# Kernel tuning notes

Measured on AMD Instinct MI355X. Metric: run time of the kernel, lower is better.

## Reference

```python
import jax, jax.numpy as jnp
import numpy as np

B, T, D = 2, 1024, 1024
H, DH = 16, 64
HD = H * DH          # head_dim = n_heads*d_head = 1024
F = 2048             # expert_dim
E = 8                # n_routed_experts


def bitlinear(x, W):
    # 1.58-bit ternary quant with straight-through estimator
    scale = jnp.clip(jnp.abs(W).mean(axis=1, keepdims=True), 1e-5, None)
    wq = jnp.clip(jnp.round(W / scale), -1.0, 1.0)
    w = W + jax.lax.stop_gradient(wq * scale - W)
    return x @ w.T


def layernorm(x, g, b):
    m = jnp.mean(x, -1, keepdims=True)
    v = jnp.mean((x - m) ** 2, -1, keepdims=True)
    return (x - m) * jax.lax.rsqrt(v + 1e-5) * g + b


def setup_inputs():
    key = jax.random.key(0)
    ks = jax.random.split(key, 12)
    n = lambda k, s, sd: jax.random.normal(k, s, jnp.float32) * sd
    return {
        'x': jax.random.normal(ks[0], (B, T, D), jnp.float32),
        'mask': jnp.tril(jnp.ones((T, T), bool))[None, None],  # causal [1,1,T,T]
        'Wq': n(ks[1], (2 * HD, D), (2 * HD) ** -0.5),
        'Wk': n(ks[2], (2 * HD, D), (2 * HD) ** -0.5),
        'Wv': n(ks[3], (HD, D), HD ** -0.5),
        'Wo': n(ks[4], (D, HD), D ** -0.5),
        'lambda_q': n(ks[5], (H, DH), 0.1),
        'lambda_k': n(ks[6], (H, DH), 0.1),
        'qn_g': jnp.ones(2 * HD), 'qn_b': jnp.zeros(2 * HD),
        'kn_g': jnp.ones(2 * HD), 'kn_b': jnp.zeros(2 * HD),
        'attn_g': jnp.ones(D), 'attn_b': jnp.zeros(D),
        'ffn_g': jnp.ones(D), 'ffn_b': jnp.zeros(D),
        'moe_g': jnp.ones(D), 'moe_b': jnp.zeros(D),
        'shared_w1': n(ks[7], (F, D), F ** -0.5),
        'shared_w2': n(ks[8], (D, F), D ** -0.5),
        'expert_w1': n(ks[9], (E, F, D), F ** -0.5),
        'expert_w2': n(ks[10], (E, D, F), D ** -0.5),
        'router_w': n(ks[11], (E, D), 0.02),
    }


def diff_attention(x, mask, Wq, Wk, Wv, Wo, lambda_q, lambda_k, qn_g, qn_b, kn_g, kn_b):
    Bq, Tq, _ = x.shape
    q = layernorm(bitlinear(x, Wq), qn_g, qn_b).reshape(Bq, Tq, 2, H, DH)
    k = layernorm(bitlinear(x, Wk), kn_g, kn_b).reshape(Bq, Tq, 2, H, DH)
    v = bitlinear(x, Wv).reshape(Bq, Tq, H, DH)
    lam = jnp.clip(jnp.exp(lambda_q.mean() - lambda_k.mean()), 0.1, 2.0)
    scale = DH ** -0.5

    def one_attn(qi, ki):
        s = jnp.einsum('bthd,bshd->bhts', qi, ki) * scale
        s = jnp.where(mask, s, -jnp.inf)
        p = jax.nn.softmax(s, -1)
        return jnp.einsum('bhts,bshd->bthd', p, v)

    out1 = one_attn(q[:, :, 0], k[:, :, 0])
    out2 = one_attn(q[:, :, 1], k[:, :, 1])
    out = (out1 - lam * out2).reshape(Bq, Tq, HD)
    return bitlinear(out, Wo)


def ignition_moe(x, moe_g, moe_b, shared_w1, shared_w2, expert_w1, expert_w2, router_w):
    h = layernorm(x, moe_g, moe_b)
    shared = bitlinear(jax.nn.silu(bitlinear(h, shared_w1)), shared_w2)
    probs = jax.nn.softmax(h @ router_w.T, -1)          # [B,T,E]
    idx = jnp.argmax(probs, -1)                          # top-1 expert id
    top_p = jnp.take_along_axis(probs, idx[..., None], -1)  # [B,T,1]
    routed = jnp.zeros_like(h)
    for e in range(E):  # small fixed expert count
        out_e = bitlinear(jax.nn.silu(bitlinear(h, expert_w1[e])), expert_w2[e])
        sel = (idx == e)[..., None]
        routed = routed + jnp.where(sel, out_e * top_p, 0.0)
    return shared + routed


def reference(x, mask, Wq, Wk, Wv, Wo, lambda_q, lambda_k, qn_g, qn_b, kn_g, kn_b,
              attn_g, attn_b, ffn_g, ffn_b, moe_g, moe_b,
              shared_w1, shared_w2, expert_w1, expert_w2, router_w):
    h = layernorm(x, attn_g, attn_b)
    x = x + diff_attention(h, mask, Wq, Wk, Wv, Wo, lambda_q, lambda_k, qn_g, qn_b, kn_g, kn_b)
    h = layernorm(x, ffn_g, ffn_b)
    x = x + ignition_moe(h, moe_g, moe_b, shared_w1, shared_w2, expert_w1, expert_w2, router_w)
    return x
```

## Files before the change

### kernel.cpp

```cpp
#include <hip/hip_runtime.h>
#include <hip/hip_bf16.h>

#define B_ 2
#define T_ 1024
#define D_ 1024
#define H_ 16
#define DH_ 64
#define F_ 2048
#define E_ 8
#define M_ 2048

typedef _Float16 half8 __attribute__((ext_vector_type(8)));
typedef _Float16 half4v __attribute__((ext_vector_type(4)));
typedef float f32x4 __attribute__((ext_vector_type(4)));

template<bool ABS>
__device__ __forceinline__ float np_pairwise_wave(const float* a, int K, int lane) {
  int nb = K >> 7;
  float s = 0.f;
  if (lane < nb) {
    const float* p = a + (lane << 7);
    float r[8];
    #pragma unroll
    for (int j = 0; j < 8; ++j) r[j] = ABS ? fabsf(p[j]) : p[j];
    for (int i = 8; i < 128; i += 8)
      #pragma unroll
      for (int j = 0; j < 8; ++j) r[j] += ABS ? fabsf(p[i + j]) : p[i + j];
    s = ((r[0] + r[1]) + (r[2] + r[3])) + ((r[4] + r[5]) + (r[6] + r[7]));
  }
  for (int off = 1; off < nb; off <<= 1) s += __shfl_xor(s, off);
  return __shfl(s, 0);
}

__global__ __launch_bounds__(64) void k_scaleq_all(
    const float* __restrict__ Wq, const float* __restrict__ Wk,
    const float* __restrict__ Wv, const float* __restrict__ Wo,
    const float* __restrict__ sw1, const float* __restrict__ sw2,
    const float* __restrict__ ew1, const float* __restrict__ ew2,
    float* __restrict__ scWq, float* __restrict__ scWk,
    float* __restrict__ scWv, float* __restrict__ scWo,
    float* __restrict__ scS1, float* __restrict__ scS2,
    float* __restrict__ scE1, float* __restrict__ scE2,
    _Float16* __restrict__ QWq, _Float16* __restrict__ QWk,
    _Float16* __restrict__ QWv, _Float16* __restrict__ QWo,
    _Float16* __restrict__ QS1, _Float16* __restrict__ QS2,
    _Float16* __restrict__ QE1, _Float16* __restrict__ QE2)
{
  int r = blockIdx.x, lane = threadIdx.x;
  const float* W; float* sc; _Float16* qo; int K; int rr;
  if      (r < 2048)  { W = Wq;  sc = scWq; qo = QWq; K = 1024; rr = r; }
  else if (r < 4096)  { W = Wk;  sc = scWk; qo = QWk; K = 1024; rr = r - 2048; }
  else if (r < 5120)  { W = Wv;  sc = scWv; qo = QWv; K = 1024; rr = r - 4096; }
  else if (r < 6144)  { W = Wo;  sc = scWo; qo = QWo; K = 1024; rr = r - 5120; }
  else if (r < 8192)  { W = sw1; sc = scS1; qo = QS1; K = 1024; rr = r - 6144; }
  else if (r < 9216)  { W = sw2; sc = scS2; qo = QS2; K = 2048; rr = r - 8192; }
  else if (r < 25600) { W = ew1; sc = scE1; qo = QE1; K = 1024; rr = r - 9216; }
  else                { W = ew2; sc = scE2; qo = QE2; K = 2048; rr = r - 25600; }
  const float* row = W + (size_t)rr * K;
  float S = np_pairwise_wave<true>(row, K, lane);
  float s = fmaxf(S / (float)K, 1e-5f);
  if (lane == 0) sc[rr] = s;
  _Float16* dst = qo + (size_t)rr * K;
  for (int k = lane * 4; k < K; k += 256) {
    float4 w = *reinterpret_cast<const float4*>(row + k);
    float wv[4] = {w.x, w.y, w.z, w.w};
    half4v q4;
    #pragma unroll
    for (int j = 0; j < 4; ++j) {
      float q = rintf(wv[j] / s);
      q = fminf(1.f, fmaxf(-1.f, q));
      q4[j] = (_Float16)q;
    }
    *reinterpret_cast<half4v*>(dst + k) = q4;
  }
}

__global__ __launch_bounds__(64) void k_lambda(const float* __restrict__ lq,
                                               const float* __restrict__ lk,
                                               float* __restrict__ lam) {
  int lane = threadIdx.x;
  float mq = np_pairwise_wave<false>(lq, 1024, lane) / 1024.0f;
  float mk = np_pairwise_wave<false>(lk, 1024, lane) / 1024.0f;
  if (lane == 0) {
    float l = expf(mq - mk);
    lam[0] = fminf(2.0f, fmaxf(0.1f, l));
  }
}

__global__ __launch_bounds__(256) void k_layernorm(const float* __restrict__ in,
                                                   const float* __restrict__ g,
                                                   const float* __restrict__ b,
                                                   float* __restrict__ out, int Dd) {
  #pragma clang fp contract(off)
  __shared__ float row[2048];
  __shared__ float sq[2048];
  __shared__ float stat[2];
  int m = blockIdx.x, tid = threadIdx.x;
  const float* src = in + (size_t)m * Dd;
  for (int d = tid; d < Dd; d += 256) row[d] = src[d];
  __syncthreads();
  if (tid < 64) {
    float S = np_pairwise_wave<false>(row, Dd, tid);
    if (tid == 0) stat[0] = S;
  }
  __syncthreads();
  float mean = stat[0] / (float)Dd;
  for (int d = tid; d < Dd; d += 256) { float t = row[d] - mean; sq[d] = t * t; }
  __syncthreads();
  if (tid < 64) {
    float S = np_pairwise_wave<false>(sq, Dd, tid);
    if (tid == 0) stat[1] = S;
  }
  __syncthreads();
  float var = stat[1] / (float)Dd;
  float rs = 1.0f / sqrtf(var + 1e-5f);
  float* dst = out + (size_t)m * Dd;
  for (int d = tid; d < Dd; d += 256) {
    float t = row[d] - mean;
    float u = t * rs;
    float v = u * g[d];
    dst[d] = v + b[d];
  }
}

__global__ __launch_bounds__(256) void k_layernorm_split(const float* __restrict__ in,
                                                         const float* __restrict__ g,
                                                         const float* __restrict__ b,
                                                         _Float16* __restrict__ oh,
                                                         _Float16* __restrict__ ol, int Dd) {
  #pragma clang fp contract(off)
  __shared__ float row[2048];
  __shared__ float sq[2048];
  __shared__ float stat[2];
  int m = blockIdx.x, tid = threadIdx.x;
  const float* src = in + (size_t)m * Dd;
  for (int d = tid; d < Dd; d += 256) row[d] = src[d];
  __syncthreads();
  if (tid < 64) {
    float S = np_pairwise_wave<false>(row, Dd, tid);
    if (tid == 0) stat[0] = S;
  }
  __syncthreads();
  float mean = stat[0] / (float)Dd;
  for (int d = tid; d < Dd; d += 256) { float t = row[d] - mean; sq[d] = t * t; }
  __syncthreads();
  if (tid < 64) {
    float S = np_pairwise_wave<false>(sq, Dd, tid);
    if (tid == 0) stat[1] = S;
  }
  __syncthreads();
  float var = stat[1] / (float)Dd;
  float rs = 1.0f / sqrtf(var + 1e-5f);
  #pragma unroll 1
  for (int d = tid; d < Dd; d += 256) {
    float t = row[d] - mean;
    float u = t * rs;
    float v = u * g[d];
    float w = v + b[d];
    _Float16 hv = (_Float16)w;
    oh[(size_t)m * Dd + d] = hv;
    ol[(size_t)m * Dd + d] = (_Float16)((w - (float)hv) * 2048.0f);
  }
}

__global__ __launch_bounds__(256) void k_lnln(const float* __restrict__ in,
                                              const float* __restrict__ g1, const float* __restrict__ b1,
                                              const float* __restrict__ g2, const float* __restrict__ b2,
                                              float* __restrict__ outf,
                                              _Float16* __restrict__ outh) {
  #pragma clang fp contract(off)
  __shared__ float row[1024];
  __shared__ float tmp[1024];
  __shared__ float stat[2];
  int m = blockIdx.x, tid = threadIdx.x;
  const float* src = in + (size_t)m * 1024;
  for (int d = tid; d < 1024; d += 256) row[d] = src[d];
  __syncthreads();
  if (tid < 64) { float S = np_pairwise_wave<false>(row, 1024, tid); if (tid == 0) stat[0] = S; }
  __syncthreads();
  float mean = stat[0] / 1024.0f;
  for (int d = tid; d < 1024; d += 256) { float t = row[d] - mean; tmp[d] = t * t; }
  __syncthreads();
  if (tid < 64) { float S = np_pairwise_wave<false>(tmp, 1024, tid); if (tid == 0) stat[1] = S; }
  __syncthreads();
  float rs = 1.0f / sqrtf(stat[1] / 1024.0f + 1e-5f);
  for (int d = tid; d < 1024; d += 256) {
    float t = row[d] - mean;
    float u = t * rs;
    float v = u * g1[d];
    tmp[d] = v + b1[d];
  }
  __syncthreads();
  if (tid < 64) { float S = np_pairwise_wave<false>(tmp, 1024, tid); if (tid == 0) stat[0] = S; }
  __syncthreads();
  float mean2 = stat[0] / 1024.0f;
  for (int d = tid; d < 1024; d += 256) { float t = tmp[d] - mean2; row[d] = t * t; }
  __syncthreads();
  if (tid < 64) { float S = np_pairwise_wave<false>(row, 1024, tid); if (tid == 0) stat[1] = S; }
  __syncthreads();
  float rs2 = 1.0f / sqrtf(stat[1] / 1024.0f + 1e-5f);
  for (int d = tid; d < 1024; d += 256) {
    float t = tmp[d] - mean2;
    float u = t * rs2;
    float v = u * g2[d];
    float w = v + b2[d];
    outf[(size_t)m * 1024 + d] = w;
    outh[(size_t)m * 1024 + d] = (_Float16)w;
  }
}

template<int EPI, int XM, int DUAL>
__global__ __launch_bounds__(256) void k_mgemm(
    const _Float16* __restrict__ Agh, const _Float16* __restrict__ Agl, int lda,
    const _Float16* __restrict__ Wh, const float* __restrict__ scf,
    float* __restrict__ Cout, _Float16* __restrict__ Ch, _Float16* __restrict__ Ch2,
    int ldc, int N, int K,
    const float* __restrict__ res, const float* __restrict__ add2,
    const int* __restrict__ offs, const int* __restrict__ tlist,
    const float* __restrict__ topp)
{
  int e = XM ? blockIdx.z : 0;
  int mbase = 0, mcount = M_;
  const float* sc = scf;
  const _Float16* Whb = Wh;
  if (XM) {
    mbase = offs[e]; mcount = offs[e + 1] - mbase;
    Whb = Wh + (size_t)e * N * K;
    sc = scf + (size_t)e * N;
  }
  int m0 = blockIdx.y * 128;
  if (XM && m0 >= mcount) return;
  int n0 = blockIdx.x * 64;

  __shared__ __align__(16) _Float16 As[4][128][8];
  __shared__ __align__(16) _Float16 Als[DUAL ? 4 : 1][128][8];
  __shared__ __align__(16) _Float16 Qs[4][64][8];

  int tid = threadIdx.x;
  int lm  = tid >> 1;
  int kcA = (tid & 1) * 16;
  int lw  = tid >> 2;
  int kcW = (tid & 3) * 8;

  int am  = m0 + lm;
  int amc = XM ? ((am < mcount) ? am : (mcount - 1)) : am;
  int arow;
  if (XM == 1)      arow = tlist[mbase + amc];
  else if (XM == 2) arow = mbase + amc;
  else              arow = am;
  const _Float16* Arh = Agh + (size_t)arow * lda;
  const _Float16* Arl = DUAL ? (Agl + (size_t)arow * lda) : nullptr;
  const _Float16* Wrh = Whb + (size_t)(n0 + lw) * K;

  int wv = tid >> 6, lane = tid & 63;
  int wm = wv >> 1, wn = wv & 1;
  int ks = lane >> 4, fr = lane & 15;

  f32x4 acch[4][2], accl[4][2];
  #pragma unroll
  for (int i = 0; i < 4; i++)
    #pragma unroll
    for (int j = 0; j < 2; j++) { acch[i][j] = (f32x4)0.f; accl[i][j] = (f32x4)0.f; }

  for (int kt = 0; kt < K; kt += 32) {
    half8 a0 = *reinterpret_cast<const half8*>(Arh + kt + kcA);
    half8 a1 = *reinterpret_cast<const half8*>(Arh + kt + kcA + 8);
    half8 b0, b1;
    if (DUAL) {
      b0 = *reinterpret_cast<const half8*>(Arl + kt + kcA);
      b1 = *reinterpret_cast<const half8*>(Arl + kt + kcA + 8);
    }
    half8 qv = *reinterpret_cast<const half8*>(Wrh + kt + kcW);
    __syncthreads();
    int sA = kcA >> 3;
    *reinterpret_cast<half8*>(&As[sA][lm][0])     = a0;
    *reinterpret_cast<half8*>(&As[sA + 1][lm][0]) = a1;
    if (DUAL) {
      *reinterpret_cast<half8*>(&Als[sA][lm][0])     = b0;
      *reinterpret_cast<half8*>(&Als[sA + 1][lm][0]) = b1;
    }
    *reinterpret_cast<half8*>(&Qs[kcW >> 3][lw][0]) = qv;
    __syncthreads();
    half8 bfr0 = *reinterpret_cast<half8*>(&Qs[ks][wn * 32 + fr][0]);
    half8 bfr1 = *reinterpret_cast<half8*>(&Qs[ks][wn * 32 + 16 + fr][0]);
    #pragma unroll
    for (int i = 0; i < 4; i++) {
      half8 ah = *reinterpret_cast<half8*>(&As[ks][wm * 64 + i * 16 + fr][0]);
      acch[i][0] = __builtin_amdgcn_mfma_f32_16x16x32_f16(ah, bfr0, acch[i][0], 0, 0, 0);
      acch[i][1] = __builtin_amdgcn_mfma_f32_16x16x32_f16(ah, bfr1, acch[i][1], 0, 0, 0);
      if (DUAL) {
        half8 al = *reinterpret_cast<half8*>(&Als[ks][wm * 64 + i * 16 + fr][0]);
        accl[i][0] = __builtin_amdgcn_mfma_f32_16x16x32_f16(al, bfr0, accl[i][0], 0, 0, 0);
        accl[i][1] = __builtin_amdgcn_mfma_f32_16x16x32_f16(al, bfr1, accl[i][1], 0, 0, 0);
      }
    }
  }

  #pragma unroll
  for (int j = 0; j < 2; j++) {
    int col = n0 + wn * 32 + j * 16 + fr;
    float scl = sc[col];
    #pragma unroll
    for (int i = 0; i < 4; i++) {
      #pragma unroll
      for (int r = 0; r < 4; r++) {
        int lrow = m0 + wm * 64 + i * 16 + ks * 4 + r;
        if (XM && lrow >= mcount) continue;
        int orow;
        if (XM == 1)      orow = mbase + lrow;
        else if (XM == 2) orow = tlist[mbase + lrow];
        else              orow = lrow;
        float v = acch[i][j][r];
        if (DUAL) v += accl[i][j][r] * (1.0f / 2048.0f);
        v *= scl;
        if (EPI == 1) {
          v = v * (1.0f / (1.0f + __expf(-v)));
          Ch[(size_t)orow * ldc + col] = (_Float16)v;
        } else if (EPI == 2) {
          Cout[(size_t)orow * ldc + col] = res[(size_t)orow * ldc + col] + v;
        } else {
          Cout[(size_t)orow * ldc + col] = v;
        }
      }
    }
  }
}

__global__ __launch_bounds__(256) void k_mgemm_qkv(
    const _Float16* __restrict__ Agh, const _Float16* __restrict__ Agl,
    const _Float16* __restrict__ WQ_, const _Float16* __restrict__ WK_, const _Float16* __restrict__ WV_,
    const float* __restrict__ scq, const float* __restrict__ sck, const float* __restrict__ scv,
    float* __restrict__ Cq, float* __restrict__ Ck,
    _Float16* __restrict__ Vth, _Float16* __restrict__ Vtl)
{
  int nt = blockIdx.x;
  int sel = (nt < 32) ? 0 : (nt < 64 ? 1 : 2);
  int n0 = ((sel == 0) ? nt : (sel == 1) ? (nt - 32) : (nt - 64)) * 64;
  const _Float16* Wh = (sel == 0) ? WQ_ : (sel == 1) ? WK_ : WV_;
  const float* sc = (sel == 0) ? scq : (sel == 1) ? sck : scv;
  int m0 = blockIdx.y * 128;

  __shared__ __align__(16) _Float16 As[4][128][8];
  __shared__ __align__(16) _Float16 Als[4][128][8];
  __shared__ __align__(16) _Float16 Qs[4][64][8];

  int tid = threadIdx.x;
  int lm  = tid >> 1;
  int kcA = (tid & 1) * 16;
  int lw  = tid >> 2;
  int kcW = (tid & 3) * 8;

  const _Float16* Arh = Agh + (size_t)(m0 + lm) * 1024;
  const _Float16* Arl = Agl + (size_t)(m0 + lm) * 1024;
  const _Float16* Wrh = Wh + (size_t)(n0 + lw) * 1024;

  int wv = tid >> 6, lane = tid & 63;
  int wm = wv >> 1, wn = wv & 1;
  int ks = lane >> 4, fr = lane & 15;

  f32x4 acch[4][2], accl[4][2];
  #pragma unroll
  for (int i = 0; i < 4; i++)
    #pragma unroll
    for (int j = 0; j < 2; j++) { acch[i][j] = (f32x4)0.f; accl[i][j] = (f32x4)0.f; }

  for (int kt = 0; kt < 1024; kt += 32) {
    half8 a0 = *reinterpret_cast<const half8*>(Arh + kt + kcA);
    half8 a1 = *reinterpret_cast<const half8*>(Arh + kt + kcA + 8);
    half8 b0 = *reinterpret_cast<const half8*>(Arl + kt + kcA);
    half8 b1 = *reinterpret_cast<const half8*>(Arl + kt + kcA + 8);
    half8 qv = *reinterpret_cast<const half8*>(Wrh + kt + kcW);
    __syncthreads();
    int sA = kcA >> 3;
    *reinterpret_cast<half8*>(&As[sA][lm][0])      = a0;
    *reinterpret_cast<half8*>(&As[sA + 1][lm][0])  = a1;
    *reinterpret_cast<half8*>(&Als[sA][lm][0])     = b0;
    *reinterpret_cast<half8*>(&Als[sA + 1][lm][0]) = b1;
    *reinterpret_cast<half8*>(&Qs[kcW >> 3][lw][0]) = qv;
    __syncthreads();
    half8 bfr0 = *reinterpret_cast<half8*>(&Qs[ks][wn * 32 + fr][0]);
    half8 bfr1 = *reinterpret_cast<half8*>(&Qs[ks][wn * 32 + 16 + fr][0]);
    #pragma unroll
    for (int i = 0; i < 4; i++) {
      half8 ah = *reinterpret_cast<half8*>(&As[ks][wm * 64 + i * 16 + fr][0]);
      half8 al = *reinterpret_cast<half8*>(&Als[ks][wm * 64 + i * 16 + fr][0]);
      acch[i][0] = __builtin_amdgcn_mfma_f32_16x16x32_f16(ah, bfr0, acch[i][0], 0, 0, 0);
      acch[i][1] = __builtin_amdgcn_mfma_f32_16x16x32_f16(ah, bfr1, acch[i][1], 0, 0, 0);
      accl[i][0] = __builtin_amdgcn_mfma_f32_16x16x32_f16(al, bfr0, accl[i][0], 0, 0, 0);
      accl[i][1] = __builtin_amdgcn_mfma_f32_16x16x32_f16(al, bfr1, accl[i][1], 0, 0, 0);
    }
  }

  #pragma unroll
  for (int j = 0; j < 2; j++) {
    int col = n0 + wn * 32 + j * 16 + fr;
    float scl = sc[col];
    #pragma unroll
    for (int i = 0; i < 4; i++) {
      #pragma unroll
      for (int r = 0; r < 4; r++) {
        int orow = m0 + wm * 64 + i * 16 + ks * 4 + r;
        float v = (acch[i][j][r] + accl[i][j][r] * (1.0f / 2048.0f)) * scl;
        if (sel == 0) {
          Cq[(size_t)orow * 2048 + col] = v;
        } else if (sel == 1) {
          Ck[(size_t)orow * 2048 + col] = v;
        } else {
          int bb = orow >> 10, tok = orow & 1023;
          size_t vidx = ((size_t)(bb << 10) + col) * 1024 + tok;
          _Float16 hv = (_Float16)v;
          Vth[vidx] = hv;
          Vtl[vidx] = (_Float16)((v - (float)hv) * 2048.0f);
        }
      }
    }
  }
}

__global__ __launch_bounds__(256) void k_mgemm_moe1(
    const _Float16* __restrict__ Agh,
    const _Float16* __restrict__ WhS, const _Float16* __restrict__ WhE,
    const float* __restrict__ scS, const float* __restrict__ scE,
    _Float16* __restrict__ CS, _Float16* __restrict__ CE,
    const int* __restrict__ offs, const int* __restrict__ tlist)
{
  int z = blockIdx.z;
  int mbase = 0, mcount = M_;
  const _Float16* Whb = WhS;
  const float* sc = scS;
  if (z > 0) {
    int e = z - 1;
    mbase = offs[e]; mcount = offs[e + 1] - mbase;
    Whb = WhE + (size_t)e * 2048 * 1024;
    sc = scE + (size_t)e * 2048;
  }
  int m0 = blockIdx.y * 128;
  if (z > 0 && m0 >= mcount) return;
  int n0 = blockIdx.x * 64;

  __shared__ __align__(16) _Float16 As[4][128][8];
  __shared__ __align__(16) _Float16 Qs[4][64][8];

  int tid = threadIdx.x;
  int lm  = tid >> 1;
  int kcA = (tid & 1) * 16;
  int lw  = tid >> 2;
  int kcW = (tid & 3) * 8;

  int am  = m0 + lm;
  int amc = (z > 0) ? ((am < mcount) ? am : (mcount - 1)) : am;
  int arow = (z > 0) ? tlist[mbase + amc] : am;
  const _Float16* Arh = Agh + (size_t)arow * 1024;
  const _Float16* Wrh = Whb + (size_t)(n0 + lw) * 1024;

  int wv = tid >> 6, lane = tid & 63;
  int wm = wv >> 1, wn = wv & 1;
  int ks = lane >> 4, fr = lane & 15;

  f32x4 acch[4][2];
  #pragma unroll
  for (int i = 0; i < 4; i++)
    #pragma unroll
    for (int j = 0; j < 2; j++) acch[i][j] = (f32x4)0.f;

  for (int kt = 0; kt < 1024; kt += 32) {
    half8 a0 = *reinterpret_cast<const half8*>(Arh + kt + kcA);
    half8 a1 = *reinterpret_cast<const half8*>(Arh + kt + kcA + 8);
    half8 qv = *reinterpret_cast<const half8*>(Wrh + kt + kcW);
    __syncthreads();
    int sA = kcA >> 3;
    *reinterpret_cast<half8*>(&As[sA][lm][0])     = a0;
    *reinterpret_cast<half8*>(&As[sA + 1][lm][0]) = a1;
    *reinterpret_cast<half8*>(&Qs[kcW >> 3][lw][0]) = qv;
    __syncthreads();
    half8 bfr0 = *reinterpret_cast<half8*>(&Qs[ks][wn * 32 + fr][0]);
    half8 bfr1 = *reinterpret_cast<half8*>(&Qs[ks][wn * 32 + 16 + fr][0]);
    #pragma unroll
    for (int i = 0; i < 4; i++) {
      half8 ah = *reinterpret_cast<half8*>(&As[ks][wm * 64 + i * 16 + fr][0]);
      acch[i][0] = __builtin_amdgcn_mfma_f32_16x16x32_f16(ah, bfr0, acch[i][0], 0, 0, 0);
      acch[i][1] = __builtin_amdgcn_mfma_f32_16x16x32_f16(ah, bfr1, acch[i][1], 0, 0, 0);
    }
  }

  #pragma unroll
  for (int j = 0; j < 2; j++) {
    int col = n0 + wn * 32 + j * 16 + fr;
    float scl = sc[col];
    #pragma unroll
    for (int i = 0; i < 4; i++) {
      #pragma unroll
      for (int r = 0; r < 4; r++) {
        int lrow = m0 + wm * 64 + i * 16 + ks * 4 + r;
        if (z > 0 && lrow >= mcount) continue;
        float v = acch[i][j][r] * scl;
        v = v * (1.0f / (1.0f + __expf(-v)));
        if (z > 0) CE[(size_t)(mbase + lrow) * 2048 + col] = (_Float16)v;
        else       CS[(size_t)lrow * 2048 + col] = (_Float16)v;
      }
    }
  }
}

__global__ __launch_bounds__(256) void k_mgemm_moe2(
    const _Float16* __restrict__ SMh, const _Float16* __restrict__ T1h,
    const _Float16* __restrict__ WhS, const _Float16* __restrict__ WhE,
    const float* __restrict__ scS, const float* __restrict__ scE,
    float* __restrict__ SO, float* __restrict__ RT,
    const int* __restrict__ offs, const int* __restrict__ tlist,
    const float* __restrict__ topp)
{
  int z = blockIdx.z;
  int mbase = 0, mcount = M_;
  const _Float16* Agh = SMh;
  const _Float16* Whb = WhS;
  const float* sc = scS;
  if (z > 0) {
    int e = z - 1;
    mbase = offs[e]; mcount = offs[e + 1] - mbase;
    Agh = T1h;
    Whb = WhE + (size_t)e * 1024 * 2048;
    sc = scE + (size_t)e * 1024;
  }
  int m0 = blockIdx.y * 128;
  if (z > 0 && m0 >= mcount) return;
  int n0 = blockIdx.x * 64;

  __shared__ __align__(16) _Float16 As[4][128][8];
  __shared__ __align__(16) _Float16 Qs[4][64][8];

  int tid = threadIdx.x;
  int lm  = tid >> 1;
  int kcA = (tid & 1) * 16;
  int lw  = tid >> 2;
  int kcW = (tid & 3) * 8;

  int am  = m0 + lm;
  int amc = (z > 0) ? ((am < mcount) ? am : (mcount - 1)) : am;
  int arow = (z > 0) ? (mbase + amc) : am;
  const _Float16* Arh = Agh + (size_t)arow * 2048;
  const _Float16* Wrh = Whb + (size_t)(n0 + lw) * 2048;

  int wv = tid >> 6, lane = tid & 63;
  int wm = wv >> 1, wn = wv & 1;
  int ks = lane >> 4, fr = lane & 15;

  f32x4 acch[4][2];
  #pragma unroll
  for (int i = 0; i < 4; i++)
    #pragma unroll
    for (int j = 0; j < 2; j++) acch[i][j] = (f32x4)0.f;

  for (int kt = 0; kt < 2048; kt += 32) {
    half8 a0 = *reinterpret_cast<const half8*>(Arh + kt + kcA);
    half8 a1 = *reinterpret_cast<const half8*>(Arh + kt + kcA + 8);
    half8 qv = *reinterpret_cast<const half8*>(Wrh + kt + kcW);
    __syncthreads();
    int sA = kcA >> 3;
    *reinterpret_cast<half8*>(&As[sA][lm][0])     = a0;
    *reinterpret_cast<half8*>(&As[sA + 1][lm][0]) = a1;
    *reinterpret_cast<half8*>(&Qs[kcW >> 3][lw][0]) = qv;
    __syncthreads();
    half8 bfr0 = *reinterpret_cast<half8*>(&Qs[ks][wn * 32 + fr][0]);
    half8 bfr1 = *reinterpret_cast<half8*>(&Qs[ks][wn * 32 + 16 + fr][0]);
    #pragma unroll
    for (int i = 0; i < 4; i++) {
      half8 ah = *reinterpret_cast<half8*>(&As[ks][wm * 64 + i * 16 + fr][0]);
      acch[i][0] = __builtin_amdgcn_mfma_f32_16x16x32_f16(ah, bfr0, acch[i][0], 0, 0, 0);
      acch[i][1] = __builtin_amdgcn_mfma_f32_16x16x32_f16(ah, bfr1, acch[i][1], 0, 0, 0);
    }
  }

  #pragma unroll
  for (int j = 0; j < 2; j++) {
    int col = n0 + wn * 32 + j * 16 + fr;
    float scl = sc[col];
    #pragma unroll
    for (int i = 0; i < 4; i++) {
      #pragma unroll
      for (int r = 0; r < 4; r++) {
        int lrow = m0 + wm * 64 + i * 16 + ks * 4 + r;
        if (z > 0 && lrow >= mcount) continue;
        float v = acch[i][j][r] * scl;
        if (z > 0) {
          int orow = tlist[mbase + lrow];
          RT[(size_t)orow * 1024 + col] = v * topp[orow];
        } else {
          SO[(size_t)lrow * 1024 + col] = v;
        }
      }
    }
  }
}

__global__ __launch_bounds__(256) void k_final(const float* __restrict__ x1,
                                               const float* __restrict__ so,
                                               const float* __restrict__ rt,
                                               float* __restrict__ out) {
  #pragma clang fp contract(off)
  int i = blockIdx.x * 256 + threadIdx.x;
  float moe = so[i] + rt[i];
  out[i] = x1[i] + moe;
}

__global__ __launch_bounds__(256) void k_attn4(const float* __restrict__ q,
                                               const _Float16* __restrict__ khg,
                                               const _Float16* __restrict__ klg,
                                               const _Float16* __restrict__ vth,
                                               const _Float16* __restrict__ vtl,
                                               const float* __restrict__ lamp,
                                               _Float16* __restrict__ aoh,
                                               _Float16* __restrict__ aol)
{
  __shared__ __align__(16) _Float16 KH[2][64][72];
  __shared__ __align__(16) _Float16 KL[2][64][72];
  __shared__ __align__(16) _Float16 VH[64][72];
  __shared__ __align__(16) _Float16 VL[64][72];
  __shared__ __align__(16) _Float16 PH[4][16][72];
  __shared__ __align__(16) _Float16 PL[4][16][72];

  int bh = blockIdx.x;
  int b = bh >> 4, h = bh & 15;
  int y = blockIdx.y;
  int tq = (y < 8) ? (2 * y) : (31 - 2 * y);
  int t0 = tq * 64;
  int tid = threadIdx.x;
  int wm = tid >> 6, lane = tid & 63;
  int ks = lane >> 4, fr = lane & 15;
  size_t tokbase = (size_t)b * T_;
  float lam = lamp[0];

  half8 qh[2][2], ql[2][2];
  {
    const float* qr = q + (tokbase + t0 + wm * 16 + fr) * 2048 + h * 64;
    #pragma unroll
    for (int g = 0; g < 2; ++g)
      #pragma unroll
      for (int s = 0; s < 2; ++s) {
        const float* p = qr + g * 1024 + s * 32 + ks * 8;
        float4 x0 = *reinterpret_cast<const float4*>(p);
        float4 x1 = *reinterpret_cast<const float4*>(p + 4);
        float xv[8] = {x0.x,x0.y,x0.z,x0.w, x1.x,x1.y,x1.z,x1.w};
        half8 hh, ll;
        #pragma unroll
        for (int j = 0; j < 8; ++j) {
          _Float16 hv = (_Float16)xv[j];
          hh[j] = hv; ll[j] = (_Float16)((xv[j] - (float)hv) * 2048.0f);
        }
        qh[g][s] = hh; ql[g][s] = ll;
      }
  }

  f32x4 Oh[2][4], Ox[2][4];
  #pragma unroll
  for (int g = 0; g < 2; ++g)
    #pragma unroll
    for (int d = 0; d < 4; ++d) { Oh[g][d] = (f32x4)0.f; Ox[g][d] = (f32x4)0.f; }
  float mrun[2][4], lrun[2][4];
  #pragma unroll
  for (int g = 0; g < 2; ++g)
    #pragma unroll
    for (int r = 0; r < 4; ++r) { mrun[g][r] = -1e30f; lrun[g][r] = 0.f; }

  int key = tid & 63;
  int d0 = (tid >> 6) * 16;
  half8 rkh[2][2], rkl[2][2], rvh[2], rvl[2];
  {
    #pragma unroll
    for (int g = 0; g < 2; ++g) {
      const _Float16* sh = khg + (size_t)(tokbase + key) * 2048 + g * 1024 + h * 64 + d0;
      const _Float16* sl = klg + (size_t)(tokbase + key) * 2048 + g * 1024 + h * 64 + d0;
      rkh[g][0] = *reinterpret_cast<const half8*>(sh);
      rkh[g][1] = *reinterpret_cast<const half8*>(sh + 8);
      rkl[g][0] = *reinterpret_cast<const half8*>(sl);
      rkl[g][1] = *reinterpret_cast<const half8*>(sl + 8);
    }
    size_t vb = ((size_t)b * 1024 + h * 64 + key) * 1024 + d0;
    rvh[0] = *reinterpret_cast<const half8*>(vth + vb);
    rvh[1] = *reinterpret_cast<const half8*>(vth + vb + 8);
    rvl[0] = *reinterpret_cast<const half8*>(vtl + vb);
    rvl[1] = *reinterpret_cast<const half8*>(vtl + vb + 8);
  }

  for (int jt = 0; jt <= tq; ++jt) {
    int kv0 = jt * 64;
    __syncthreads();
    #pragma unroll
    for (int g = 0; g < 2; ++g) {
      *reinterpret_cast<half8*>(&KH[g][key][d0])     = rkh[g][0];
      *reinterpret_cast<half8*>(&KH[g][key][d0 + 8]) = rkh[g][1];
      *reinterpret_cast<half8*>(&KL[g][key][d0])     = rkl[g][0];
      *reinterpret_cast<half8*>(&KL[g][key][d0 + 8]) = rkl[g][1];
    }
    *reinterpret_cast<half8*>(&VH[key][d0])     = rvh[0];
    *reinterpret_cast<half8*>(&VH[key][d0 + 8]) = rvh[1];
    *reinterpret_cast<half8*>(&VL[key][d0])     = rvl[0];
    *reinterpret_cast<half8*>(&VL[key][d0 + 8]) = rvl[1];
    if (jt < tq) {
      int nv0 = kv0 + 64;
      #pragma unroll
      for (int g = 0; g < 2; ++g) {
        const _Float16* sh = khg + (size_t)(tokbase + nv0 + key) * 2048 + g * 1024 + h * 64 + d0;
        const _Float16* sl = klg + (size_t)(tokbase + nv0 + key) * 2048 + g * 1024 + h * 64 + d0;
        rkh[g][0] = *reinterpret_cast<const half8*>(sh);
        rkh[g][1] = *reinterpret_cast<const half8*>(sh + 8);
        rkl[g][0] = *reinterpret_cast<const half8*>(sl);
        rkl[g][1] = *reinterpret_cast<const half8*>(sl + 8);
      }
      size_t vb = ((size_t)b * 1024 + h * 64 + key) * 1024 + nv0 + d0;
      rvh[0] = *reinterpret_cast<const half8*>(vth + vb);
      rvh[1] = *reinterpret_cast<const half8*>(vth + vb + 8);
      rvl[0] = *reinterpret_cast<const half8*>(vtl + vb);
      rvl[1] = *reinterpret_cast<const half8*>(vtl + vb + 8);
    }
    __syncthreads();

    bool diag = (jt == tq);
    #pragma unroll
    for (int g = 0; g < 2; ++g) {
      f32x4 Sh[4], Sx[4];
      #pragma unroll
      for (int kf = 0; kf < 4; ++kf) { Sh[kf] = (f32x4)0.f; Sx[kf] = (f32x4)0.f; }
      #pragma unroll
      for (int s = 0; s < 2; ++s) {
        #pragma unroll
        for (int kf = 0; kf < 4; ++kf) {
          half8 kh = *reinterpret_cast<half8*>(&KH[g][kf * 16 + fr][s * 32 + ks * 8]);
          half8 kl = *reinterpret_cast<half8*>(&KL[g][kf * 16 + fr][s * 32 + ks * 8]);
          Sh[kf] = __builtin_amdgcn_mfma_f32_16x16x32_f16(qh[g][s], kh, Sh[kf], 0, 0, 0);
          Sx[kf] = __builtin_amdgcn_mfma_f32_16x16x32_f16(qh[g][s], kl, Sx[kf], 0, 0, 0);
          Sx[kf] = __builtin_amdgcn_mfma_f32_16x16x32_f16(ql[g][s], kh, Sx[kf], 0, 0, 0);
        }
      }
      float sv[4][4];
      #pragma unroll
      for (int kf = 0; kf < 4; ++kf)
        #pragma unroll
        for (int r = 0; r < 4; ++r) {
          float s_ = (Sh[kf][r] + Sx[kf][r] * (1.0f / 2048.0f)) * 0.125f;
          if (diag) {
            int row_abs = t0 + wm * 16 + ks * 4 + r;
            int col_abs = kv0 + kf * 16 + fr;
            if (col_abs > row_abs) s_ = -1e30f;
          }
          sv[kf][r] = s_;
        }
      #pragma unroll
      for (int r = 0; r < 4; ++r) {
        float tmax = fmaxf(fmaxf(sv[0][r], sv[1][r]), fmaxf(sv[2][r], sv[3][r]));
        #pragma unroll
        for (int msk = 1; msk < 16; msk <<= 1) tmax = fmaxf(tmax, __shfl_xor(tmax, msk));
        bool up = tmax > mrun[g][r];
        float mnew = up ? tmax : mrun[g][r];
        float e0 = __expf(sv[0][r] - mnew);
        float e1 = __expf(sv[1][r] - mnew);
        float e2 = __expf(sv[2][r] - mnew);
        float e3 = __expf(sv[3][r] - mnew);
        float rsum = (e0 + e1) + (e2 + e3);
        #pragma unroll
        for (int msk = 1; msk < 16; msk <<= 1) rsum += __shfl_xor(rsum, msk);
        if (up) {
          float scale = __expf(mrun[g][r] - tmax);
          lrun[g][r] = lrun[g][r] * scale + rsum;
          mrun[g][r] = tmax;
          #pragma unroll
          for (int df = 0; df < 4; ++df) { Oh[g][df][r] *= scale; Ox[g][df][r] *= scale; }
        } else {
          lrun[g][r] += rsum;
        }
        float ev[4] = {e0, e1, e2, e3};
        #pragma unroll
        for (int kf = 0; kf < 4; ++kf) {
          _Float16 ph = (_Float16)ev[kf];
          _Float16 pl = (_Float16)((ev[kf] - (float)ph) * 2048.0f);
          PH[wm][ks * 4 + r][kf * 16 + fr] = ph;
          PL[wm][ks * 4 + r][kf * 16 + fr] = pl;
        }
      }
      #pragma unroll
      for (int s = 0; s < 2; ++s) {
        half8 pah = *reinterpret_cast<half8*>(&PH[wm][fr][s * 32 + ks * 8]);
        half8 pal = *reinterpret_cast<half8*>(&PL[wm][fr][s * 32 + ks * 8]);
        #pragma unroll
        for (int df = 0; df < 4; ++df) {
          half8 vh = *reinterpret_cast<half8*>(&VH[df * 16 + fr][s * 32 + ks * 8]);
          half8 vl = *reinterpret_cast<half8*>(&VL[df * 16 + fr][s * 32 + ks * 8]);
          Oh[g][df] = __builtin_amdgcn_mfma_f32_16x16x32_f16(pah, vh, Oh[g][df], 0, 0, 0);
          Ox[g][df] = __builtin_amdgcn_mfma_f32_16x16x32_f16(pah, vl, Ox[g][df], 0, 0, 0);
          Ox[g][df] = __builtin_amdgcn_mfma_f32_16x16x32_f16(pal, vh, Ox[g][df], 0, 0, 0);
        }
      }
    }
  }

  #pragma unroll
  for (int df = 0; df < 4; ++df) {
    #pragma unroll
    for (int r = 0; r < 4; ++r) {
      int row_abs = t0 + wm * 16 + ks * 4 + r;
      int d = df * 16 + fr;
      float o1 = (Oh[0][df][r] + Ox[0][df][r] * (1.0f / 2048.0f)) / lrun[0][r];
      float o2 = (Oh[1][df][r] + Ox[1][df][r] * (1.0f / 2048.0f)) / lrun[1][r];
      float oo = o1 - lam * o2;
      size_t idx = (tokbase + row_abs) * 1024 + h * 64 + d;
      _Float16 hv = (_Float16)oo;
      aoh[idx] = hv;
      aol[idx] = (_Float16)((oo - (float)hv) * 2048.0f);
    }
  }
}

__global__ __launch_bounds__(256) void k_router(const float* __restrict__ hm,
                                                const float* __restrict__ rw,
                                                int* __restrict__ idx,
                                                float* __restrict__ topp)
{
  #pragma clang fp contract(off)
  int tid = threadIdx.x;
  int tg = tid >> 3, e = tid & 7;
  int m = blockIdx.x * 32 + tg;
  const float* hr = hm + (size_t)m * 1024;
  const float* wr = rw + (size_t)e * 1024;
  float l = 0.f;
  for (int dd = 0; dd < 1024; ++dd) l = __builtin_fmaf(hr[dd], wr[dd], l);
  float mx = l;
  #pragma unroll
  for (int off = 1; off < 8; off <<= 1) mx = fmaxf(mx, __shfl_xor(mx, off, 8));
  float p = __expf(l - mx);
  float den = p;
  #pragma unroll
  for (int off = 1; off < 8; off <<= 1) den += __shfl_xor(den, off, 8);
  float prob = p / den;
  float pm = prob;
  #pragma unroll
  for (int off = 1; off < 8; off <<= 1) pm = fmaxf(pm, __shfl_xor(pm, off, 8));
  unsigned long long ball = __ballot(prob == pm);
  int grp = (tid & 63) >> 3;
  int first = __ffsll((unsigned long long)((ball >> (grp * 8)) & 0xFFull)) - 1;
  if (e == 0) { idx[m] = first; topp[m] = pm; }
}

__global__ __launch_bounds__(512) void k_route_fill(const int* __restrict__ idx,
                                                    int* __restrict__ offs,
                                                    int* __restrict__ tlist)
{
  __shared__ int cnt[8];
  __shared__ int off[9];
  int w = threadIdx.x >> 6, lane = threadIdx.x & 63;
  int total = 0;
  for (int it = 0; it < M_ / 64; ++it) {
    int tok = it * 64 + lane;
    unsigned long long m = __ballot(idx[tok] == w);
    total += __popcll(m);
  }
  if (lane == 0) cnt[w] = total;
  __syncthreads();
  if (threadIdx.x == 0) {
    int o = 0;
    for (int e = 0; e < 8; ++e) { off[e] = o; o += cnt[e]; }
    off[8] = o;
    for (int e = 0; e < 9; ++e) offs[e] = off[e];
  }
  __syncthreads();
  int base = off[w];
  for (int it = 0; it < M_ / 64; ++it) {
    int tok = it * 64 + lane;
    bool sel = (idx[tok] == w);
    unsigned long long m = __ballot(sel);
    if (sel) {
      int pos = base + __popcll(m & ((1ull << lane) - 1ull));
      tlist[pos] = tok;
    }
    base += __popcll(m);
  }
}

extern "C" void kernel_launch(void* const* d_in, const int* in_sizes, int n_in,
                              void* d_out, int out_size, void* d_ws, size_t ws_size,
                              hipStream_t stream) {
  const float* x   = (const float*)d_in[0];
  const float* Wq  = (const float*)d_in[2];
  const float* Wk  = (const float*)d_in[3];
  const float* Wv  = (const float*)d_in[4];
  const float* Wo  = (const float*)d_in[5];
  const float* lq  = (const float*)d_in[6];
  const float* lk  = (const float*)d_in[7];
  const float* qng = (const float*)d_in[8];
  const float* qnb = (const float*)d_in[9];
  const float* kng = (const float*)d_in[10];
  const float* knb = (const float*)d_in[11];
  const float* ag  = (const float*)d_in[12];
  const float* ab  = (const float*)d_in[13];
  const float* fg  = (const float*)d_in[14];
  const float* fb  = (const float*)d_in[15];
  const float* mg  = (const float*)d_in[16];
  const float* mb  = (const float*)d_in[17];
  const float* sw1 = (const float*)d_in[18];
  const float* sw2 = (const float*)d_in[19];
  const float* ew1 = (const float*)d_in[20];
  const float* ew2 = (const float*)d_in[21];
  const float* rw  = (const float*)d_in[22];

  float* ws = (float*)d_ws;
  size_t o = 0;
  float* scWq = ws + o; o += 2048;
  float* scWk = ws + o; o += 2048;
  float* scWv = ws + o; o += 1024;
  float* scWo = ws + o; o += 1024;
  float* scS1 = ws + o; o += 2048;
  float* scS2 = ws + o; o += 1024;
  float* scE1 = ws + o; o += 8 * 2048;
  float* scE2 = ws + o; o += 8 * 1024;
  float* lam  = ws + o; o += 16;
  float* TOPP = ws + o; o += 2048;
  int*   IDX  = (int*)(ws + o); o += 2048;
  int*   OFFS = (int*)(ws + o); o += 16;
  int*   TLIST= (int*)(ws + o); o += 2048;
  o = (o + 15) & ~(size_t)15;

  _Float16* QWq = (_Float16*)(ws + o); o += 1024 * 1024;
  _Float16* QWk = (_Float16*)(ws + o); o += 1024 * 1024;
  _Float16* QWv = (_Float16*)(ws + o); o += 512 * 1024;
  _Float16* QWo = (_Float16*)(ws + o); o += 512 * 1024;
  _Float16* QS1 = (_Float16*)(ws + o); o += 1024 * 1024;
  _Float16* QS2 = (_Float16*)(ws + o); o += 1024 * 1024;
  _Float16* QE1 = (_Float16*)(ws + o); o += 8 * 1024 * 1024;
  _Float16* QE2 = (_Float16*)(ws + o); o += 8 * 1024 * 1024;

  float* RA = ws + o; o += 2 * 1024 * 1024;
  _Float16* H1h = (_Float16*)RA;
  _Float16* H1l = (_Float16*)(RA + 1024 * 1024);
  _Float16* SMh = (_Float16*)RA;
  float* RB = ws + o; o += 2 * 1024 * 1024;
  _Float16* AOh = (_Float16*)RB;
  _Float16* AOl = (_Float16*)(RB + 1024 * 1024);
  _Float16* HMh = (_Float16*)RB;
  _Float16* T1h = (_Float16*)(ws + o); o += 2 * 1024 * 1024;

  const size_t MQ = (size_t)M_ * 2048;
  float* QP = ws + o; o += MQ;
  float* KP = ws + o; o += MQ;
  _Float16* KHg = (_Float16*)(ws + o); o += 2 * 1024 * 1024;
  _Float16* KLg = (_Float16*)(ws + o); o += 2 * 1024 * 1024;
  _Float16* VTH = (_Float16*)(ws + o); o += 1024 * 1024;
  _Float16* VTL = (_Float16*)(ws + o); o += 1024 * 1024;

  float* X1 = QP;
  float* HM = QP + MQ / 2;
  float* SO = KP;
  float* RT = (float*)KHg;

  k_scaleq_all<<<33792, 64, 0, stream>>>(Wq, Wk, Wv, Wo, sw1, sw2, ew1, ew2,
                                         scWq, scWk, scWv, scWo, scS1, scS2, scE1, scE2,
                                         QWq, QWk, QWv, QWo, QS1, QS2, QE1, QE2);
  k_lambda<<<1, 64, 0, stream>>>(lq, lk, lam);

  k_layernorm_split<<<M_, 256, 0, stream>>>(x, ag, ab, H1h, H1l, 1024);
  k_mgemm_qkv<<<dim3(80,16), 256, 0, stream>>>(H1h, H1l, QWq, QWk, QWv, scWq, scWk, scWv, QP, KP, VTH, VTL);
  k_layernorm<<<M_, 256, 0, stream>>>(QP, qng, qnb, QP, 2048);
  k_layernorm_split<<<M_, 256, 0, stream>>>(KP, kng, knb, KHg, KLg, 2048);
  k_attn4<<<dim3(32, 16), 256, 0, stream>>>(QP, KHg, KLg, VTH, VTL, lam, AOh, AOl);
  k_mgemm<2,0,1><<<dim3(16,16), 256, 0, stream>>>(AOh, AOl, 1024, QWo, scWo, X1, nullptr, nullptr, 1024, 1024, 1024, x, nullptr, nullptr, nullptr, nullptr);

  k_lnln<<<M_, 256, 0, stream>>>(X1, fg, fb, mg, mb, HM, HMh);
  k_router<<<M_ / 32, 256, 0, stream>>>(HM, rw, IDX, TOPP);
  k_route_fill<<<1, 512, 0, stream>>>(IDX, OFFS, TLIST);

  k_mgemm_moe1<<<dim3(32,16,9), 256, 0, stream>>>(HMh, QS1, QE1, scS1, scE1, SMh, T1h, OFFS, TLIST);
  k_mgemm_moe2<<<dim3(16,16,9), 256, 0, stream>>>(SMh, T1h, QS2, QE2, scS2, scE2, SO, RT, OFFS, TLIST, TOPP);

  k_final<<<8192, 256, 0, stream>>>(X1, SO, RT, (float*)d_out);
}
```

Before: 539.8 us.

## Widen MoE GEMM N-tile to 128 and fuse small launches

The MoE GEMM kernels now compute a 128-column tile per block instead of 64. Each A tile loaded into shared memory is reused across twice as many MFMAs, and the grid is halved accordingly. The lambda computation is folded into the weight quantization kernel as an extra block, and the Q and K layernorms are merged into one launch. This cuts redundant A loads and launch overhead, at the cost of more accumulator registers and fewer blocks, which may lower occupancy.

```diff
diff --git a/kernel.cpp b/kernel.cpp
--- a/kernel.cpp
+++ b/kernel.cpp
@@ -37,6 +37,7 @@
     const float* __restrict__ Wv, const float* __restrict__ Wo,
     const float* __restrict__ sw1, const float* __restrict__ sw2,
     const float* __restrict__ ew1, const float* __restrict__ ew2,
+    const float* __restrict__ lq, const float* __restrict__ lk,
     float* __restrict__ scWq, float* __restrict__ scWk,
     float* __restrict__ scWv, float* __restrict__ scWo,
     float* __restrict__ scS1, float* __restrict__ scS2,
@@ -44,9 +45,19 @@
     _Float16* __restrict__ QWq, _Float16* __restrict__ QWk,
     _Float16* __restrict__ QWv, _Float16* __restrict__ QWo,
     _Float16* __restrict__ QS1, _Float16* __restrict__ QS2,
-    _Float16* __restrict__ QE1, _Float16* __restrict__ QE2)
+    _Float16* __restrict__ QE1, _Float16* __restrict__ QE2,
+    float* __restrict__ lam)
 {
   int r = blockIdx.x, lane = threadIdx.x;
+  if (r == 33792) {
+    float mq = np_pairwise_wave<false>(lq, 1024, lane) / 1024.0f;
+    float mk = np_pairwise_wave<false>(lk, 1024, lane) / 1024.0f;
+    if (lane == 0) {
+      float l = expf(mq - mk);
+      lam[0] = fminf(2.0f, fmaxf(0.1f, l));
+    }
+    return;
+  }
   const float* W; float* sc; _Float16* qo; int K; int rr;
   if      (r < 2048)  { W = Wq;  sc = scWq; qo = QWq; K = 1024; rr = r; }
   else if (r < 4096)  { W = Wk;  sc = scWk; qo = QWk; K = 1024; rr = r - 2048; }
@@ -75,54 +86,6 @@
   }
 }
 
-__global__ __launch_bounds__(64) void k_lambda(const float* __restrict__ lq,
-                                               const float* __restrict__ lk,
-                                               float* __restrict__ lam) {
-  int lane = threadIdx.x;
-  float mq = np_pairwise_wave<false>(lq, 1024, lane) / 1024.0f;
-  float mk = np_pairwise_wave<false>(lk, 1024, lane) / 1024.0f;
-  if (lane == 0) {
-    float l = expf(mq - mk);
-    lam[0] = fminf(2.0f, fmaxf(0.1f, l));
-  }
-}
-
-__global__ __launch_bounds__(256) void k_layernorm(const float* __restrict__ in,
-                                                   const float* __restrict__ g,
-                                                   const float* __restrict__ b,
-                                                   float* __restrict__ out, int Dd) {
-  #pragma clang fp contract(off)
-  __shared__ float row[2048];
-  __shared__ float sq[2048];
-  __shared__ float stat[2];
-  int m = blockIdx.x, tid = threadIdx.x;
-  const float* src = in + (size_t)m * Dd;
-  for (int d = tid; d < Dd; d += 256) row[d] = src[d];
-  __syncthreads();
-  if (tid < 64) {
-    float S = np_pairwise_wave<false>(row, Dd, tid);
-    if (tid == 0) stat[0] = S;
-  }
-  __syncthreads();
-  float mean = stat[0] / (float)Dd;
-  for (int d = tid; d < Dd; d += 256) { float t = row[d] - mean; sq[d] = t * t; }
-  __syncthreads();
-  if (tid < 64) {
-    float S = np_pairwise_wave<false>(sq, Dd, tid);
-    if (tid == 0) stat[1] = S;
-  }
-  __syncthreads();
-  float var = stat[1] / (float)Dd;
-  float rs = 1.0f / sqrtf(var + 1e-5f);
-  float* dst = out + (size_t)m * Dd;
-  for (int d = tid; d < Dd; d += 256) {
-    float t = row[d] - mean;
-    float u = t * rs;
-    float v = u * g[d];
-    dst[d] = v + b[d];
-  }
-}
-
 __global__ __launch_bounds__(256) void k_layernorm_split(const float* __restrict__ in,
                                                          const float* __restrict__ g,
                                                          const float* __restrict__ b,
@@ -160,6 +123,58 @@
     _Float16 hv = (_Float16)w;
     oh[(size_t)m * Dd + d] = hv;
     ol[(size_t)m * Dd + d] = (_Float16)((w - (float)hv) * 2048.0f);
+  }
+}
+
+__global__ __launch_bounds__(256) void k_lnqk(float* __restrict__ QP,
+                                              const float* __restrict__ qg, const float* __restrict__ qb,
+                                              const float* __restrict__ KP,
+                                              const float* __restrict__ kg, const float* __restrict__ kb,
+                                              _Float16* __restrict__ khg, _Float16* __restrict__ klg) {
+  #pragma clang fp contract(off)
+  __shared__ float row[2048];
+  __shared__ float sq[2048];
+  __shared__ float stat[2];
+  int blk = blockIdx.x, tid = threadIdx.x;
+  bool isQ = blk < 2048;
+  int m = isQ ? blk : (blk - 2048);
+  const float* src = (isQ ? (const float*)QP : KP) + (size_t)m * 2048;
+  for (int d = tid; d < 2048; d += 256) row[d] = src[d];
+  __syncthreads();
+  if (tid < 64) {
+    float S = np_pairwise_wave<false>(row, 2048, tid);
+    if (tid == 0) stat[0] = S;
+  }
+  __syncthreads();
+  float mean = stat[0] / 2048.0f;
+  for (int d = tid; d < 2048; d += 256) { float t = row[d] - mean; sq[d] = t * t; }
+  __syncthreads();
+  if (tid < 64) {
+    float S = np_pairwise_wave<false>(sq, 2048, tid);
+    if (tid == 0) stat[1] = S;
+  }
+  __syncthreads();
+  float var = stat[1] / 2048.0f;
+  float rs = 1.0f / sqrtf(var + 1e-5f);
+  if (isQ) {
+    float* dst = QP + (size_t)m * 2048;
+    for (int d = tid; d < 2048; d += 256) {
+      float t = row[d] - mean;
+      float u = t * rs;
+      float v = u * qg[d];
+      dst[d] = v + qb[d];
+    }
+  } else {
+    #pragma unroll 1
+    for (int d = tid; d < 2048; d += 256) {
+      float t = row[d] - mean;
+      float u = t * rs;
+      float v = u * kg[d];
+      float w = v + kb[d];
+      _Float16 hv = (_Float16)w;
+      khg[(size_t)m * 2048 + d] = hv;
+      klg[(size_t)m * 2048 + d] = (_Float16)((w - (float)hv) * 2048.0f);
+    }
   }
 }
 
@@ -436,10 +451,10 @@
   }
   int m0 = blockIdx.y * 128;
   if (z > 0 && m0 >= mcount) return;
-  int n0 = blockIdx.x * 64;
+  int n0 = blockIdx.x * 128;
 
   __shared__ __align__(16) _Float16 As[4][128][8];
-  __shared__ __align__(16) _Float16 Qs[4][64][8];
+  __shared__ __align__(16) _Float16 Qs[2][4][64][8];
 
   int tid = threadIdx.x;
   int lm  = tid >> 1;
@@ -451,52 +466,67 @@
   int amc = (z > 0) ? ((am < mcount) ? am : (mcount - 1)) : am;
   int arow = (z > 0) ? tlist[mbase + amc] : am;
   const _Float16* Arh = Agh + (size_t)arow * 1024;
-  const _Float16* Wrh = Whb + (size_t)(n0 + lw) * 1024;
+  const _Float16* Wr0 = Whb + (size_t)(n0 + lw) * 1024;
+  const _Float16* Wr1 = Whb + (size_t)(n0 + 64 + lw) * 1024;
 
   int wv = tid >> 6, lane = tid & 63;
   int wm = wv >> 1, wn = wv & 1;
   int ks = lane >> 4, fr = lane & 15;
 
-  f32x4 acch[4][2];
-  #pragma unroll
-  for (int i = 0; i < 4; i++)
-    #pragma unroll
-    for (int j = 0; j < 2; j++) acch[i][j] = (f32x4)0.f;
+  f32x4 acch[2][4][2];
+  #pragma unroll
+  for (int nt = 0; nt < 2; nt++)
+    #pragma unroll
+    for (int i = 0; i < 4; i++)
+      #pragma unroll
+      for (int j = 0; j < 2; j++) acch[nt][i][j] = (f32x4)0.f;
 
   for (int kt = 0; kt < 1024; kt += 32) {
     half8 a0 = *reinterpret_cast<const half8*>(Arh + kt + kcA);
     half8 a1 = *reinterpret_cast<const half8*>(Arh + kt + kcA + 8);
-    half8 qv = *reinterpret_cast<const half8*>(Wrh + kt + kcW);
+    half8 q0 = *reinterpret_cast<const half8*>(Wr0 + kt + kcW);
+    half8 q1 = *reinterpret_cast<const half8*>(Wr1 + kt + kcW);
     __syncthreads();
     int sA = kcA >> 3;
     *reinterpret_cast<half8*>(&As[sA][lm][0])     = a0;
     *reinterpret_cast<half8*>(&As[sA + 1][lm][0]) = a1;
-    *reinterpret_cast<half8*>(&Qs[kcW >> 3][lw][0]) = qv;
+    *reinterpret_cast<half8*>(&Qs[0][kcW >> 3][lw][0]) = q0;
+    *reinterpret_cast<half8*>(&Qs[1][kcW >> 3][lw][0]) = q1;
     __syncthreads();
-    half8 bfr0 = *reinterpret_cast<half8*>(&Qs[ks][wn * 32 + fr][0]);
-    half8 bfr1 = *reinterpret_cast<half8*>(&Qs[ks][wn * 32 + 16 + fr][0]);
+    half8 bf[2][2];
+    #pragma unroll
+    for (int nt = 0; nt < 2; nt++) {
+      bf[nt][0] = *reinterpret_cast<half8*>(&Qs[nt][ks][wn * 32 + fr][0]);
+      bf[nt][1] = *reinterpret_cast<half8*>(&Qs[nt][ks][wn * 32 + 16 + fr][0]);
+    }
     #pragma unroll
     for (int i = 0; i < 4; i++) {
       half8 ah = *reinterpret_cast<half8*>(&As[ks][wm * 64 + i * 16 + fr][0]);
-      acch[i][0] = __builtin_amdgcn_mfma_f32_16x16x32_f16(ah, bfr0, acch[i][0], 0, 0, 0);
-      acch[i][1] = __builtin_amdgcn_mfma_f32_16x16x32_f16(ah, bfr1, acch[i][1], 0, 0, 0);
-    }
-  }
-
-  #pragma unroll
-  for (int j = 0; j < 2; j++) {
-    int col = n0 + wn * 32 + j * 16 + fr;
-    float scl = sc[col];
-    #pragma unroll
-    for (int i = 0; i < 4; i++) {
-      #pragma unroll
-      for (int r = 0; r < 4; r++) {
-        int lrow = m0 + wm * 64 + i * 16 + ks * 4 + r;
-        if (z > 0 && lrow >= mcount) continue;
-        float v = acch[i][j][r] * scl;
-        v = v * (1.0f / (1.0f + __expf(-v)));
-        if (z > 0) CE[(size_t)(mbase + lrow) * 2048 + col] = (_Float16)v;
-        else       CS[(size_t)lrow * 2048 + col] = (_Float16)v;
+      #pragma unroll
+      for (int nt = 0; nt < 2; nt++) {
+        acch[nt][i][0] = __builtin_amdgcn_mfma_f32_16x16x32_f16(ah, bf[nt][0], acch[nt][i][0], 0, 0, 0);
+        acch[nt][i][1] = __builtin_amdgcn_mfma_f32_16x16x32_f16(ah, bf[nt][1], acch[nt][i][1], 0, 0, 0);
+      }
+    }
+  }
+
+  #pragma unroll
+  for (int nt = 0; nt < 2; nt++) {
+    #pragma unroll
+    for (int j = 0; j < 2; j++) {
+      int col = n0 + nt * 64 + wn * 32 + j * 16 + fr;
+      float scl = sc[col];
+      #pragma unroll
+      for (int i = 0; i < 4; i++) {
+        #pragma unroll
+        for (int r = 0; r < 4; r++) {
+          int lrow = m0 + wm * 64 + i * 16 + ks * 4 + r;
+          if (z > 0 && lrow >= mcount) continue;
+          float v = acch[nt][i][j][r] * scl;
+          v = v * (1.0f / (1.0f + __expf(-v)));
+          if (z > 0) CE[(size_t)(mbase + lrow) * 2048 + col] = (_Float16)v;
+          else       CS[(size_t)lrow * 2048 + col] = (_Float16)v;
+        }
       }
     }
   }
@@ -524,10 +554,10 @@
   }
   int m0 = blockIdx.y * 128;
   if (z > 0 && m0 >= mcount) return;
-  int n0 = blockIdx.x * 64;
+  int n0 = blockIdx.x * 128;
 
   __shared__ __align__(16) _Float16 As[4][128][8];
-  __shared__ __align__(16) _Float16 Qs[4][64][8];
+  __shared__ __align__(16) _Float16 Qs[2][4][64][8];
 
   int tid = threadIdx.x;
   int lm  = tid >> 1;
@@ -539,54 +569,69 @@
   int amc = (z > 0) ? ((am < mcount) ? am : (mcount - 1)) : am;
   int arow = (z > 0) ? (mbase + amc) : am;
   const _Float16* Arh = Agh + (size_t)arow * 2048;
-  const _Float16* Wrh = Whb + (size_t)(n0 + lw) * 2048;
+  const _Float16* Wr0 = Whb + (size_t)(n0 + lw) * 2048;
+  const _Float16* Wr1 = Whb + (size_t)(n0 + 64 + lw) * 2048;
 
   int wv = tid >> 6, lane = tid & 63;
   int wm = wv >> 1, wn = wv & 1;
   int ks = lane >> 4, fr = lane & 15;
 
-  f32x4 acch[4][2];
-  #pragma unroll
-  for (int i = 0; i < 4; i++)
-    #pragma unroll
-    for (int j = 0; j < 2; j++) acch[i][j] = (f32x4)0.f;
+  f32x4 acch[2][4][2];
+  #pragma unroll
+  for (int nt = 0; nt < 2; nt++)
+    #pragma unroll
+    for (int i = 0; i < 4; i++)
+      #pragma unroll
+      for (int j = 0; j < 2; j++) acch[nt][i][j] = (f32x4)0.f;
 
   for (int kt = 0; kt < 2048; kt += 32) {
     half8 a0 = *reinterpret_cast<const half8*>(Arh + kt + kcA);
     half8 a1 = *reinterpret_cast<const half8*>(Arh + kt + kcA + 8);
-    half8 qv = *reinterpret_cast<const half8*>(Wrh + kt + kcW);
+    half8 q0 = *reinterpret_cast<const half8*>(Wr0 + kt + kcW);
+    half8 q1 = *reinterpret_cast<const half8*>(Wr1 + kt + kcW);
     __syncthreads();
     int sA = kcA >> 3;
     *reinterpret_cast<half8*>(&As[sA][lm][0])     = a0;
     *reinterpret_cast<half8*>(&As[sA + 1][lm][0]) = a1;
-    *reinterpret_cast<half8*>(&Qs[kcW >> 3][lw][0]) = qv;
+    *reinterpret_cast<half8*>(&Qs[0][kcW >> 3][lw][0]) = q0;
+    *reinterpret_cast<half8*>(&Qs[1][kcW >> 3][lw][0]) = q1;
     __syncthreads();
-    half8 bfr0 = *reinterpret_cast<half8*>(&Qs[ks][wn * 32 + fr][0]);
-    half8 bfr1 = *reinterpret_cast<half8*>(&Qs[ks][wn * 32 + 16 + fr][0]);
+    half8 bf[2][2];
+    #pragma unroll
+    for (int nt = 0; nt < 2; nt++) {
+      bf[nt][0] = *reinterpret_cast<half8*>(&Qs[nt][ks][wn * 32 + fr][0]);
+      bf[nt][1] = *reinterpret_cast<half8*>(&Qs[nt][ks][wn * 32 + 16 + fr][0]);
+    }
     #pragma unroll
     for (int i = 0; i < 4; i++) {
       half8 ah = *reinterpret_cast<half8*>(&As[ks][wm * 64 + i * 16 + fr][0]);
-      acch[i][0] = __builtin_amdgcn_mfma_f32_16x16x32_f16(ah, bfr0, acch[i][0], 0, 0, 0);
-      acch[i][1] = __builtin_amdgcn_mfma_f32_16x16x32_f16(ah, bfr1, acch[i][1], 0, 0, 0);
-    }
-  }
-
-  #pragma unroll
-  for (int j = 0; j < 2; j++) {
-    int col = n0 + wn * 32 + j * 16 + fr;
-    float scl = sc[col];
-    #pragma unroll
-    for (int i = 0; i < 4; i++) {
-      #pragma unroll
-      for (int r = 0; r < 4; r++) {
-        int lrow = m0 + wm * 64 + i * 16 + ks * 4 + r;
-        if (z > 0 && lrow >= mcount) continue;
-        float v = acch[i][j][r] * scl;
-        if (z > 0) {
-          int orow = tlist[mbase + lrow];
-          RT[(size_t)orow * 1024 + col] = v * topp[orow];
-        } else {
-          SO[(size_t)lrow * 1024 + col] = v;
+      #pragma unroll
+      for (int nt = 0; nt < 2; nt++) {
+        acch[nt][i][0] = __builtin_amdgcn_mfma_f32_16x16x32_f16(ah, bf[nt][0], acch[nt][i][0], 0, 0, 0);
+        acch[nt][i][1] = __builtin_amdgcn_mfma_f32_16x16x32_f16(ah, bf[nt][1], acch[nt][i][1], 0, 0, 0);
+      }
+    }
+  }
+
+  #pragma unroll
+  for (int nt = 0; nt < 2; nt++) {
+    #pragma unroll
+    for (int j = 0; j < 2; j++) {
+      int col = n0 + nt * 64 + wn * 32 + j * 16 + fr;
+      float scl = sc[col];
+      #pragma unroll
+      for (int i = 0; i < 4; i++) {
+        #pragma unroll
+        for (int r = 0; r < 4; r++) {
+          int lrow = m0 + wm * 64 + i * 16 + ks * 4 + r;
+          if (z > 0 && lrow >= mcount) continue;
+          float v = acch[nt][i][j][r] * scl;
+          if (z > 0) {
+            int orow = tlist[mbase + lrow];
+            RT[(size_t)orow * 1024 + col] = v * topp[orow];
+          } else {
+            SO[(size_t)lrow * 1024 + col] = v;
+          }
         }
       }
     }
@@ -950,15 +995,13 @@
   float* SO = KP;
   float* RT = (float*)KHg;
 
-  k_scaleq_all<<<33792, 64, 0, stream>>>(Wq, Wk, Wv, Wo, sw1, sw2, ew1, ew2,
+  k_scaleq_all<<<33793, 64, 0, stream>>>(Wq, Wk, Wv, Wo, sw1, sw2, ew1, ew2, lq, lk,
                                          scWq, scWk, scWv, scWo, scS1, scS2, scE1, scE2,
-                                         QWq, QWk, QWv, QWo, QS1, QS2, QE1, QE2);
-  k_lambda<<<1, 64, 0, stream>>>(lq, lk, lam);
+                                         QWq, QWk, QWv, QWo, QS1, QS2, QE1, QE2, lam);
 
   k_layernorm_split<<<M_, 256, 0, stream>>>(x, ag, ab, H1h, H1l, 1024);
   k_mgemm_qkv<<<dim3(80,16), 256, 0, stream>>>(H1h, H1l, QWq, QWk, QWv, scWq, scWk, scWv, QP, KP, VTH, VTL);
-  k_layernorm<<<M_, 256, 0, stream>>>(QP, qng, qnb, QP, 2048);
-  k_layernorm_split<<<M_, 256, 0, stream>>>(KP, kng, knb, KHg, KLg, 2048);
+  k_lnqk<<<2 * M_, 256, 0, stream>>>(QP, qng, qnb, KP, kng, knb, KHg, KLg);
   k_attn4<<<dim3(32, 16), 256, 0, stream>>>(QP, KHg, KLg, VTH, VTL, lam, AOh, AOl);
   k_mgemm<2,0,1><<<dim3(16,16), 256, 0, stream>>>(AOh, AOl, 1024, QWo, scWo, X1, nullptr, nullptr, 1024, 1024, 1024, x, nullptr, nullptr, nullptr, nullptr);
 
@@ -966,8 +1009,8 @@
   k_router<<<M_ / 32, 256, 0, stream>>>(HM, rw, IDX, TOPP);
   k_route_fill<<<1, 512, 0, stream>>>(IDX, OFFS, TLIST);
 
-  k_mgemm_moe1<<<dim3(32,16,9), 256, 0, stream>>>(HMh, QS1, QE1, scS1, scE1, SMh, T1h, OFFS, TLIST);
-  k_mgemm_moe2<<<dim3(16,16,9), 256, 0, stream>>>(SMh, T1h, QS2, QE2, scS2, scE2, SO, RT, OFFS, TLIST, TOPP);
+  k_mgemm_moe1<<<dim3(16,16,9), 256, 0, stream>>>(HMh, QS1, QE1, scS1, scE1, SMh, T1h, OFFS, TLIST);
+  k_mgemm_moe2<<<dim3(8,16,9), 256, 0, stream>>>(SMh, T1h, QS2, QE2, scS2, scE2, SO, RT, OFFS, TLIST, TOPP);
 
   k_final<<<8192, 256, 0, stream>>>(X1, SO, RT, (float*)d_out);
 }
```

Result: slower. 579.9 us (+7.4%).
